# Performance work log

Measured on AMD Instinct MI355X. Metric: run time of the kernel, lower is better.

Reference implementation:

```python
import jax, jax.numpy as jnp
import numpy as np

IN_CH = 64
OUT_CH = 64
SEQ_LEN = 2048
MODES = 64  # modes2 = min(modes1, seq_len//2) = 64
SCALE = 1.0 / (IN_CH * OUT_CH)


def setup_inputs() -> dict:
    key = jax.random.key(0)
    k1, k2, k3 = jax.random.split(key, 3)
    x = jax.random.normal(k1, (32, 8, IN_CH, SEQ_LEN), dtype=jnp.float32)
    # torch.rand(...) complex init scaled by 1/(in*out): real & imag in [0, scale)
    wr = SCALE * jax.random.uniform(k2, (IN_CH, OUT_CH, MODES), dtype=jnp.float32)
    wi = SCALE * jax.random.uniform(k3, (IN_CH, OUT_CH, MODES), dtype=jnp.float32)
    return {"x": x, "wr": wr, "wi": wi}


def reference(x, wr, wi):
    # x: [B, H, E, N] real; weights complex [in, out, modes]
    N = x.shape[-1]
    w = jax.lax.complex(wr, wi)
    x_ft = jnp.fft.rfft(x)                       # [B, H, E, N//2+1] complex64
    a = x_ft[..., :MODES]                        # keep only low modes
    out_low = jnp.einsum('bjix,iox->bjox', a, w)  # per-mode complex matmul
    # zero-fill remaining frequency bins (equivalent to out_ft zeros + slice set)
    pad = N // 2 + 1 - MODES
    out_ft = jnp.pad(out_low, ((0, 0), (0, 0), (0, 0), (0, pad)))
    return jnp.fft.irfft(out_ft, n=N)            # [B, H, out_ch, N] real
```

## Files before the change

### kernel.cpp

```cpp
#include <hip/hip_runtime.h>
#include <hip/hip_bf16.h>


typedef __bf16 bf16x8 __attribute__((ext_vector_type(8)));
typedef float  f32x4  __attribute__((ext_vector_type(4)));

#define SEQ 2048
#define NM2 128
#define KS  2
#define TWO_PI_OVER_N 3.0679615757712823e-03f

__device__ __forceinline__ unsigned int rnbf(float f) {
  unsigned int u = __builtin_bit_cast(unsigned int, f);
  return (u + 0x7fffu + ((u >> 16) & 1u)) >> 16;
}
__device__ __forceinline__ unsigned int pack2(float a, float b) {
  return rnbf(a) | (rnbf(b) << 16);
}
__device__ __forceinline__ float frombf(unsigned int lo16_in_place) {
  return __builtin_bit_cast(float, lo16_in_place);
}

typedef const __attribute__((address_space(1))) unsigned int gu32;
typedef __attribute__((address_space(3))) unsigned int lu32;

__global__ __launch_bounds__(256) void k_tables(unsigned short* __restrict__ t1sw,
                                                unsigned short* __restrict__ t2t) {
  int idx = blockIdx.x * 256 + threadIdx.x;
  int c = idx >> 11;
  int n = idx & 2047;
  int k = c & 63;
  float ph = (float)((k * n) & 2047) * TWO_PI_OVER_N;
  float s, co;
  sincosf(ph, &s, &co);
  float v1 = (c < 64) ? co : -s;
  float ck = (k == 0 ? 1.0f : 2.0f) * (1.0f / 2048.0f);
  float v2 = (c < 64) ? ck * co : -ck * s;
  int kt = n >> 6, part = (n >> 3) & 7, e = n & 7;
  unsigned off = (unsigned)kt * 16384u +
                 (((unsigned)(c * 128 + part * 16)) ^ (((unsigned)c & 7u) << 4)) + 2u * (unsigned)e;
  *(unsigned short*)((char*)t1sw + off) = (unsigned short)rnbf(v1);
  t2t[n * NM2 + c] = (unsigned short)rnbf(v2);
}

__global__ __launch_bounds__(256) void k_gemm1(const float* __restrict__ x,
                                               const unsigned short* __restrict__ t1sw,
                                               unsigned short* __restrict__ P) {
  __shared__ int4 lds4[65536 / 16];
  char* lds = (char*)lds4;
  const int tid = threadIdx.x, wave = tid >> 6, lane = tid & 63;
  const int mtile = blockIdx.x >> 1, ks = blockIdx.x & (KS - 1);
  const int r0 = mtile * 64;
  const int kbase = ks * (SEQ / KS);
  const char* t1base = (const char*)t1sw + (size_t)(kbase >> 6) * 16384;

  const float* xsrc[4];
#pragma unroll
  for (int p = 0; p < 4; ++p) {
    const int row = p * 16 + wave * 4 + (lane >> 4);
    const int u = (lane & 15) ^ (row & 7);
    xsrc[p] = x + (size_t)(r0 + row) * SEQ + kbase + u * 4;
  }

  f32x4 acc[8] = {};

#pragma unroll
  for (int p = 0; p < 4; ++p)
    __builtin_amdgcn_global_load_lds((gu32*)(xsrc[p]),
                                     (lu32*)(lds + p * 4096 + wave * 1024), 16, 0, 0);
#pragma unroll
  for (int p = 0; p < 4; ++p)
    __builtin_amdgcn_global_load_lds((gu32*)(t1base + (p * 256 + tid) * 16),
                                     (lu32*)(lds + 32768 + (p * 256 + wave * 64) * 16), 16, 0, 0);
  asm volatile("s_waitcnt vmcnt(0)" ::: "memory");
  __builtin_amdgcn_s_barrier();

  const int a = wave * 16 + (lane & 15);
  const unsigned xra = (unsigned)(a & 7) << 4;
  const int kg = lane >> 4;

  for (int it = 0; it < 16; ++it) {
    const int cur = it & 1, nxt = cur ^ 1;
    const int xoff = cur * 16384;
    const int toff = 32768 + cur * 16384;
    if (it < 15) {
      const char* tg = t1base + (it + 1) * 16384;
#pragma unroll
      for (int p = 0; p < 4; ++p)
        __builtin_amdgcn_global_load_lds((gu32*)(xsrc[p] + (it + 1) * 64),
                                         (lu32*)(lds + nxt * 16384 + p * 4096 + wave * 1024),
                                         16, 0, 0);
#pragma unroll
      for (int p = 0; p < 4; ++p)
        __builtin_amdgcn_global_load_lds((gu32*)(tg + (p * 256 + tid) * 16),
                                         (lu32*)(lds + 32768 + nxt * 16384 + (p * 256 + wave * 64) * 16),
                                         16, 0, 0);
    }
#pragma unroll
    for (int kss = 0; kss < 2; ++kss) {
      const unsigned byte0 = (unsigned)(a * 256 + kss * 128 + kg * 32);
      const f32x4 lo = *(const f32x4*)(lds + xoff + (byte0 ^ xra));
      const f32x4 hi = *(const f32x4*)(lds + xoff + ((byte0 + 16) ^ xra));
      unsigned c0, c1, c2, c3;
      asm("v_cvt_pk_bf16_f32 %0, %1, %2" : "=v"(c0) : "v"(lo[0]), "v"(lo[1]));
      asm("v_cvt_pk_bf16_f32 %0, %1, %2" : "=v"(c1) : "v"(lo[2]), "v"(lo[3]));
      asm("v_cvt_pk_bf16_f32 %0, %1, %2" : "=v"(c2) : "v"(hi[0]), "v"(hi[1]));
      asm("v_cvt_pk_bf16_f32 %0, %1, %2" : "=v"(c3) : "v"(hi[2]), "v"(hi[3]));
      uint4 pk; pk.x = c0; pk.y = c1; pk.z = c2; pk.w = c3;
      const bf16x8 av = __builtin_bit_cast(bf16x8, pk);
#pragma unroll
      for (int t = 0; t < 8; ++t) {
        const int col = t * 16 + (lane & 15);
        const bf16x8 bv = *(const bf16x8*)(lds + toff +
            ((col * 128 + kss * 64 + kg * 16) ^ ((unsigned)(col & 7) << 4)));
        acc[t] = __builtin_amdgcn_mfma_f32_16x16x32_bf16(av, bv, acc[t], 0, 0, 0);
      }
    }
    asm volatile("s_waitcnt vmcnt(0)" ::: "memory");
    __builtin_amdgcn_s_barrier();
  }
  unsigned short* Pout = P + (size_t)ks * (16384 * NM2);
#pragma unroll
  for (int t = 0; t < 8; ++t) {
    const int col = t * 16 + (lane & 15);
#pragma unroll
    for (int j = 0; j < 4; ++j) {
      const int row = r0 + wave * 16 + (lane >> 4) * 4 + j;
      Pout[row * NM2 + col] = (unsigned short)rnbf(acc[t][j]);
    }
  }
}

__global__ __launch_bounds__(256) void k_stage2(const unsigned short* __restrict__ P,
                                                const float* __restrict__ wr,
                                                const float* __restrict__ wi,
                                                unsigned short* __restrict__ Bx) {
  __shared__ float sA[4][64][64];
  const int b = blockIdx.x;
  const int bjc = b >> 2, oh = (b >> 1) & 1, kh = b & 1;
  const int k0 = kh * 32;
  const int tid = threadIdx.x;
#pragma unroll
  for (int p = 0; p < 16; ++p) {
    int fidx = tid + 256 * p;
    int row_lin = fidx >> 4, q = fidx & 15;
    int col = (q < 8) ? (k0 + q * 4) : (64 + k0 + (q - 8) * 4);
    const unsigned short* base = P + (size_t)(bjc * 256 + row_lin) * NM2 + col;
    f32x4 v = {};
#pragma unroll
    for (int s = 0; s < KS; ++s) {
      uint2 u = *(const uint2*)(base + (size_t)s * (16384 * NM2));
      v[0] += frombf(u.x << 16);
      v[1] += frombf(u.x & 0xffff0000u);
      v[2] += frombf(u.y << 16);
      v[3] += frombf(u.y & 0xffff0000u);
    }
    *(f32x4*)(&sA[row_lin >> 6][row_lin & 63][q * 4]) = v;
  }
  __syncthreads();
  const int o_l = tid >> 3, kg = tid & 7;
  const int o = oh * 32 + o_l;
  const int kb = k0 + kg * 4;
  f32x4 accr[4] = {};
  f32x4 acci[4] = {};
  for (int i = 0; i < 64; ++i) {
    f32x4 wrv = *(const f32x4*)(wr + (i * 64 + o) * 64 + kb);
    f32x4 wiv = *(const f32x4*)(wi + (i * 64 + o) * 64 + kb);
#pragma unroll
    for (int bj = 0; bj < 4; ++bj) {
      f32x4 ar = *(const f32x4*)(&sA[bj][i][kg * 4]);
      f32x4 ai = *(const f32x4*)(&sA[bj][i][32 + kg * 4]);
#pragma unroll
      for (int kk = 0; kk < 4; ++kk) {
        accr[bj][kk] += ar[kk] * wrv[kk] - ai[kk] * wiv[kk];
        acci[bj][kk] += ar[kk] * wiv[kk] + ai[kk] * wrv[kk];
      }
    }
  }
#pragma unroll
  for (int bj = 0; bj < 4; ++bj) {
    const int r = (bjc * 4 + bj) * 64 + o;
    uint2 vr; vr.x = pack2(accr[bj][0], accr[bj][1]); vr.y = pack2(accr[bj][2], accr[bj][3]);
    uint2 vi; vi.x = pack2(acci[bj][0], acci[bj][1]); vi.y = pack2(acci[bj][2], acci[bj][3]);
    *(uint2*)(Bx + r * NM2 + kb)      = vr;
    *(uint2*)(Bx + r * NM2 + 64 + kb) = vi;
  }
}

__global__ __launch_bounds__(256) void k_gemm2(const unsigned short* __restrict__ Bx,
                                               const unsigned short* __restrict__ t2t,
                                               float* __restrict__ out) {
  __shared__ int4 lds4[65536 / 16];
  char* lds = (char*)lds4;
  const int tid = threadIdx.x, wave = tid >> 6, lane = tid & 63;
  const int swz = (blockIdx.x & 7) * 256 + (blockIdx.x >> 3);
  const int mb = swz >> 4, nb = swz & 15;
  const int r0 = mb * 128, n0 = nb * 128;
#pragma unroll
  for (int p = 0; p < 8; ++p) {
    int seg = tid + 256 * p;
    int row = seg >> 4, part = seg & 15;
    unsigned sw = (unsigned)((row * 256 + part * 16) ^ ((row & 7) << 4));
    int4 va = *(const int4*)(Bx + (r0 + row) * NM2 + part * 8);
    *(int4*)(lds + sw) = va;
    int4 vb = *(const int4*)(t2t + (n0 + row) * NM2 + part * 8);
    *(int4*)(lds + 32768 + sw) = vb;
  }
  __syncthreads();
  f32x4 acc[2][8] = {};
#pragma unroll
  for (int ks = 0; ks < 4; ++ks) {
    const int ar0 = wave * 32 + (lane & 15);
    const int ar1 = ar0 + 16;
    const int koff = ks * 64 + (lane >> 4) * 16;
    bf16x8 a0 = *(const bf16x8*)(lds + ((ar0 * 256 + koff) ^ ((unsigned)(ar0 & 7) << 4)));
    bf16x8 a1 = *(const bf16x8*)(lds + ((ar1 * 256 + koff) ^ ((unsigned)(ar1 & 7) << 4)));
#pragma unroll
    for (int t = 0; t < 8; ++t) {
      const int col = t * 16 + (lane & 15);
      bf16x8 bv = *(const bf16x8*)(lds + 32768 + ((col * 256 + koff) ^ ((unsigned)(col & 7) << 4)));
      acc[0][t] = __builtin_amdgcn_mfma_f32_16x16x32_bf16(a0, bv, acc[0][t], 0, 0, 0);
      acc[1][t] = __builtin_amdgcn_mfma_f32_16x16x32_bf16(a1, bv, acc[1][t], 0, 0, 0);
    }
  }
#pragma unroll
  for (int m = 0; m < 2; ++m) {
#pragma unroll
    for (int j = 0; j < 4; ++j) {
      const int row = r0 + wave * 32 + m * 16 + (lane >> 4) * 4 + j;
#pragma unroll
      for (int t = 0; t < 8; ++t) {
        const int col = n0 + t * 16 + (lane & 15);
        out[row * SEQ + col] = acc[m][t][j];
      }
    }
  }
}

extern "C" void kernel_launch(void* const* d_in, const int* in_sizes, int n_in,
                              void* d_out, int out_size, void* d_ws, size_t ws_size,
                              hipStream_t stream) {
  const float* x  = (const float*)d_in[0];
  const float* wr = (const float*)d_in[1];
  const float* wi = (const float*)d_in[2];
  float* out = (float*)d_out;
  char* ws = (char*)d_ws;
  unsigned short* t1sw = (unsigned short*)(ws);
  unsigned short* t2t  = (unsigned short*)(ws + 524288);
  unsigned short* P    = (unsigned short*)(ws + 1048576);
  unsigned short* Bx   = (unsigned short*)(ws + 1048576 + (size_t)KS * 16384 * NM2 * 2);

  k_tables<<<dim3(1024), dim3(256), 0, stream>>>(t1sw, t2t);
  k_gemm1 <<<dim3(256 * KS), dim3(256), 0, stream>>>(x, t1sw, P);
  k_stage2<<<dim3(256),  dim3(256), 0, stream>>>(P, wr, wi, Bx);
  k_gemm2 <<<dim3(2048), dim3(256), 0, stream>>>(Bx, t2t, out);
}
```

Before: 89.93 us.

## Drop split-K in DFT GEMM, retile to 32-row blocks, vectorize output stores

The forward DFT GEMM no longer splits K into two partial products. Each block now covers 32 rows over the full sequence, and the four waves are arranged 2x2, so stage2 reads one bf16 partial instead of summing two and writes less intermediate data. The MFMA operands are swapped so accumulators come out transposed, which allows packed 8-byte stores in gemm1 and 16-byte float4 stores in gemm2 instead of scalar stores. The table kernel uses the hardware v_sin/v_cos instructions on revolutions and writes both cos and sin entries per thread, with half the launch size. Stage2 now runs twice as many blocks, each doing half the work. The hardware sin/cos may be slightly less accurate than sincosf.

```diff
diff --git a/kernel.cpp b/kernel.cpp
--- a/kernel.cpp
+++ b/kernel.cpp
@@ -7,8 +7,6 @@
 
 #define SEQ 2048
 #define NM2 128
-#define KS  2
-#define TWO_PI_OVER_N 3.0679615757712823e-03f
 
 __device__ __forceinline__ unsigned int rnbf(float f) {
   unsigned int u = __builtin_bit_cast(unsigned int, f);
@@ -27,73 +25,73 @@
 __global__ __launch_bounds__(256) void k_tables(unsigned short* __restrict__ t1sw,
                                                 unsigned short* __restrict__ t2t) {
   int idx = blockIdx.x * 256 + threadIdx.x;
-  int c = idx >> 11;
+  int k = idx >> 11;
   int n = idx & 2047;
-  int k = c & 63;
-  float ph = (float)((k * n) & 2047) * TWO_PI_OVER_N;
+  float rev = (float)((k * n) & 2047) * (1.0f / 2048.0f);
   float s, co;
-  sincosf(ph, &s, &co);
-  float v1 = (c < 64) ? co : -s;
+  asm("v_sin_f32 %0, %1" : "=v"(s)  : "v"(rev));
+  asm("v_cos_f32 %0, %1" : "=v"(co) : "v"(rev));
   float ck = (k == 0 ? 1.0f : 2.0f) * (1.0f / 2048.0f);
-  float v2 = (c < 64) ? ck * co : -ck * s;
   int kt = n >> 6, part = (n >> 3) & 7, e = n & 7;
-  unsigned off = (unsigned)kt * 16384u +
-                 (((unsigned)(c * 128 + part * 16)) ^ (((unsigned)c & 7u) << 4)) + 2u * (unsigned)e;
-  *(unsigned short*)((char*)t1sw + off) = (unsigned short)rnbf(v1);
-  t2t[n * NM2 + c] = (unsigned short)rnbf(v2);
+  unsigned base = (unsigned)kt * 16384u + 2u * (unsigned)e;
+  unsigned offc = base + (((unsigned)(k * 128 + part * 16)) ^ (((unsigned)k & 7u) << 4));
+  int c2 = k + 64;
+  unsigned offs = base + (((unsigned)(c2 * 128 + part * 16)) ^ (((unsigned)c2 & 7u) << 4));
+  *(unsigned short*)((char*)t1sw + offc) = (unsigned short)rnbf(co);
+  *(unsigned short*)((char*)t1sw + offs) = (unsigned short)rnbf(-s);
+  t2t[n * NM2 + k]      = (unsigned short)rnbf(ck * co);
+  t2t[n * NM2 + k + 64] = (unsigned short)rnbf(-ck * s);
 }
 
 __global__ __launch_bounds__(256) void k_gemm1(const float* __restrict__ x,
                                                const unsigned short* __restrict__ t1sw,
-                                               unsigned short* __restrict__ P) {
-  __shared__ int4 lds4[65536 / 16];
+                                               unsigned short* __restrict__ A) {
+  __shared__ int4 lds4[49152 / 16];
   char* lds = (char*)lds4;
   const int tid = threadIdx.x, wave = tid >> 6, lane = tid & 63;
-  const int mtile = blockIdx.x >> 1, ks = blockIdx.x & (KS - 1);
-  const int r0 = mtile * 64;
-  const int kbase = ks * (SEQ / KS);
-  const char* t1base = (const char*)t1sw + (size_t)(kbase >> 6) * 16384;
-
-  const float* xsrc[4];
-#pragma unroll
-  for (int p = 0; p < 4; ++p) {
+  const int r0 = blockIdx.x * 32;
+
+  const float* xsrc[2];
+#pragma unroll
+  for (int p = 0; p < 2; ++p) {
     const int row = p * 16 + wave * 4 + (lane >> 4);
     const int u = (lane & 15) ^ (row & 7);
-    xsrc[p] = x + (size_t)(r0 + row) * SEQ + kbase + u * 4;
-  }
-
-  f32x4 acc[8] = {};
-
-#pragma unroll
-  for (int p = 0; p < 4; ++p)
+    xsrc[p] = x + (size_t)(r0 + row) * SEQ + u * 4;
+  }
+
+  f32x4 acc[4] = {};
+
+#pragma unroll
+  for (int p = 0; p < 2; ++p)
     __builtin_amdgcn_global_load_lds((gu32*)(xsrc[p]),
                                      (lu32*)(lds + p * 4096 + wave * 1024), 16, 0, 0);
 #pragma unroll
   for (int p = 0; p < 4; ++p)
-    __builtin_amdgcn_global_load_lds((gu32*)(t1base + (p * 256 + tid) * 16),
-                                     (lu32*)(lds + 32768 + (p * 256 + wave * 64) * 16), 16, 0, 0);
+    __builtin_amdgcn_global_load_lds((gu32*)((const char*)t1sw + (p * 256 + tid) * 16),
+                                     (lu32*)(lds + 16384 + p * 4096 + wave * 1024), 16, 0, 0);
   asm volatile("s_waitcnt vmcnt(0)" ::: "memory");
   __builtin_amdgcn_s_barrier();
 
-  const int a = wave * 16 + (lane & 15);
+  const int wr = wave >> 1, wc = wave & 1;
+  const int a = wr * 16 + (lane & 15);
   const unsigned xra = (unsigned)(a & 7) << 4;
   const int kg = lane >> 4;
 
-  for (int it = 0; it < 16; ++it) {
+  for (int it = 0; it < 32; ++it) {
     const int cur = it & 1, nxt = cur ^ 1;
-    const int xoff = cur * 16384;
-    const int toff = 32768 + cur * 16384;
-    if (it < 15) {
-      const char* tg = t1base + (it + 1) * 16384;
-#pragma unroll
-      for (int p = 0; p < 4; ++p)
+    const int xoff = cur * 8192;
+    const int toff = 16384 + cur * 16384;
+    if (it < 31) {
+      const char* tg = (const char*)t1sw + (size_t)(it + 1) * 16384;
+#pragma unroll
+      for (int p = 0; p < 2; ++p)
         __builtin_amdgcn_global_load_lds((gu32*)(xsrc[p] + (it + 1) * 64),
-                                         (lu32*)(lds + nxt * 16384 + p * 4096 + wave * 1024),
+                                         (lu32*)(lds + nxt * 8192 + p * 4096 + wave * 1024),
                                          16, 0, 0);
 #pragma unroll
       for (int p = 0; p < 4; ++p)
         __builtin_amdgcn_global_load_lds((gu32*)(tg + (p * 256 + tid) * 16),
-                                         (lu32*)(lds + 32768 + nxt * 16384 + (p * 256 + wave * 64) * 16),
+                                         (lu32*)(lds + 16384 + nxt * 16384 + p * 4096 + wave * 1024),
                                          16, 0, 0);
     }
 #pragma unroll
@@ -109,65 +107,59 @@
       uint4 pk; pk.x = c0; pk.y = c1; pk.z = c2; pk.w = c3;
       const bf16x8 av = __builtin_bit_cast(bf16x8, pk);
 #pragma unroll
-      for (int t = 0; t < 8; ++t) {
-        const int col = t * 16 + (lane & 15);
+      for (int t = 0; t < 4; ++t) {
+        const int col = wc * 64 + t * 16 + (lane & 15);
         const bf16x8 bv = *(const bf16x8*)(lds + toff +
             ((col * 128 + kss * 64 + kg * 16) ^ ((unsigned)(col & 7) << 4)));
-        acc[t] = __builtin_amdgcn_mfma_f32_16x16x32_bf16(av, bv, acc[t], 0, 0, 0);
+        acc[t] = __builtin_amdgcn_mfma_f32_16x16x32_bf16(bv, av, acc[t], 0, 0, 0);
       }
     }
     asm volatile("s_waitcnt vmcnt(0)" ::: "memory");
     __builtin_amdgcn_s_barrier();
   }
-  unsigned short* Pout = P + (size_t)ks * (16384 * NM2);
-#pragma unroll
-  for (int t = 0; t < 8; ++t) {
-    const int col = t * 16 + (lane & 15);
-#pragma unroll
-    for (int j = 0; j < 4; ++j) {
-      const int row = r0 + wave * 16 + (lane >> 4) * 4 + j;
-      Pout[row * NM2 + col] = (unsigned short)rnbf(acc[t][j]);
-    }
-  }
-}
-
-__global__ __launch_bounds__(256) void k_stage2(const unsigned short* __restrict__ P,
+  const int row = r0 + wr * 16 + (lane & 15);
+#pragma unroll
+  for (int t = 0; t < 4; ++t) {
+    const int col0 = wc * 64 + t * 16 + kg * 4;
+    uint2 v; v.x = pack2(acc[t][0], acc[t][1]); v.y = pack2(acc[t][2], acc[t][3]);
+    *(uint2*)(A + (size_t)row * NM2 + col0) = v;
+  }
+}
+
+__global__ __launch_bounds__(256) void k_stage2(const unsigned short* __restrict__ A,
                                                 const float* __restrict__ wr,
                                                 const float* __restrict__ wi,
                                                 unsigned short* __restrict__ Bx) {
-  __shared__ float sA[4][64][64];
+  __shared__ float sA[2][64][64];
   const int b = blockIdx.x;
   const int bjc = b >> 2, oh = (b >> 1) & 1, kh = b & 1;
   const int k0 = kh * 32;
   const int tid = threadIdx.x;
 #pragma unroll
-  for (int p = 0; p < 16; ++p) {
+  for (int p = 0; p < 8; ++p) {
     int fidx = tid + 256 * p;
-    int row_lin = fidx >> 4, q = fidx & 15;
-    int col = (q < 8) ? (k0 + q * 4) : (64 + k0 + (q - 8) * 4);
-    const unsigned short* base = P + (size_t)(bjc * 256 + row_lin) * NM2 + col;
-    f32x4 v = {};
-#pragma unroll
-    for (int s = 0; s < KS; ++s) {
-      uint2 u = *(const uint2*)(base + (size_t)s * (16384 * NM2));
-      v[0] += frombf(u.x << 16);
-      v[1] += frombf(u.x & 0xffff0000u);
-      v[2] += frombf(u.y << 16);
-      v[3] += frombf(u.y & 0xffff0000u);
-    }
-    *(f32x4*)(&sA[row_lin >> 6][row_lin & 63][q * 4]) = v;
+    int row = fidx >> 4, q = fidx & 15;
+    int colbf = (q < 8) ? (k0 + q * 4) : (64 + k0 + (q - 8) * 4);
+    uint2 u = *(const uint2*)(A + (size_t)(bjc * 128 + row) * NM2 + colbf);
+    f32x4 v;
+    v[0] = frombf(u.x << 16);
+    v[1] = frombf(u.x & 0xffff0000u);
+    v[2] = frombf(u.y << 16);
+    v[3] = frombf(u.y & 0xffff0000u);
+    int dcol = (q < 8) ? q * 4 : 32 + (q - 8) * 4;
+    *(f32x4*)(&sA[row >> 6][row & 63][dcol]) = v;
   }
   __syncthreads();
-  const int o_l = tid >> 3, kg = tid & 7;
-  const int o = oh * 32 + o_l;
+  const int o = oh * 32 + (tid >> 3);
+  const int kg = tid & 7;
   const int kb = k0 + kg * 4;
-  f32x4 accr[4] = {};
-  f32x4 acci[4] = {};
+  f32x4 accr[2] = {};
+  f32x4 acci[2] = {};
   for (int i = 0; i < 64; ++i) {
     f32x4 wrv = *(const f32x4*)(wr + (i * 64 + o) * 64 + kb);
     f32x4 wiv = *(const f32x4*)(wi + (i * 64 + o) * 64 + kb);
 #pragma unroll
-    for (int bj = 0; bj < 4; ++bj) {
+    for (int bj = 0; bj < 2; ++bj) {
       f32x4 ar = *(const f32x4*)(&sA[bj][i][kg * 4]);
       f32x4 ai = *(const f32x4*)(&sA[bj][i][32 + kg * 4]);
 #pragma unroll
@@ -178,12 +170,12 @@
     }
   }
 #pragma unroll
-  for (int bj = 0; bj < 4; ++bj) {
-    const int r = (bjc * 4 + bj) * 64 + o;
+  for (int bj = 0; bj < 2; ++bj) {
+    const int r = (bjc * 2 + bj) * 64 + o;
     uint2 vr; vr.x = pack2(accr[bj][0], accr[bj][1]); vr.y = pack2(accr[bj][2], accr[bj][3]);
     uint2 vi; vi.x = pack2(acci[bj][0], acci[bj][1]); vi.y = pack2(acci[bj][2], acci[bj][3]);
-    *(uint2*)(Bx + r * NM2 + kb)      = vr;
-    *(uint2*)(Bx + r * NM2 + 64 + kb) = vi;
+    *(uint2*)(Bx + (size_t)r * NM2 + kb)      = vr;
+    *(uint2*)(Bx + (size_t)r * NM2 + 64 + kb) = vi;
   }
 }
 
@@ -201,9 +193,9 @@
     int seg = tid + 256 * p;
     int row = seg >> 4, part = seg & 15;
     unsigned sw = (unsigned)((row * 256 + part * 16) ^ ((row & 7) << 4));
-    int4 va = *(const int4*)(Bx + (r0 + row) * NM2 + part * 8);
+    int4 va = *(const int4*)(Bx + (size_t)(r0 + row) * NM2 + part * 8);
     *(int4*)(lds + sw) = va;
-    int4 vb = *(const int4*)(t2t + (n0 + row) * NM2 + part * 8);
+    int4 vb = *(const int4*)(t2t + (size_t)(n0 + row) * NM2 + part * 8);
     *(int4*)(lds + 32768 + sw) = vb;
   }
   __syncthreads();
@@ -219,20 +211,17 @@
     for (int t = 0; t < 8; ++t) {
       const int col = t * 16 + (lane & 15);
       bf16x8 bv = *(const bf16x8*)(lds + 32768 + ((col * 256 + koff) ^ ((unsigned)(col & 7) << 4)));
-      acc[0][t] = __builtin_amdgcn_mfma_f32_16x16x32_bf16(a0, bv, acc[0][t], 0, 0, 0);
-      acc[1][t] = __builtin_amdgcn_mfma_f32_16x16x32_bf16(a1, bv, acc[1][t], 0, 0, 0);
+      acc[0][t] = __builtin_amdgcn_mfma_f32_16x16x32_bf16(bv, a0, acc[0][t], 0, 0, 0);
+      acc[1][t] = __builtin_amdgcn_mfma_f32_16x16x32_bf16(bv, a1, acc[1][t], 0, 0, 0);
     }
   }
 #pragma unroll
   for (int m = 0; m < 2; ++m) {
-#pragma unroll
-    for (int j = 0; j < 4; ++j) {
-      const int row = r0 + wave * 32 + m * 16 + (lane >> 4) * 4 + j;
-#pragma unroll
-      for (int t = 0; t < 8; ++t) {
-        const int col = n0 + t * 16 + (lane & 15);
-        out[row * SEQ + col] = acc[m][t][j];
-      }
+    const int row = r0 + wave * 32 + m * 16 + (lane & 15);
+#pragma unroll
+    for (int t = 0; t < 8; ++t) {
+      const int col = n0 + t * 16 + (lane >> 4) * 4;
+      *(f32x4*)(out + (size_t)row * SEQ + col) = acc[m][t];
     }
   }
 }
@@ -247,11 +236,11 @@
   char* ws = (char*)d_ws;
   unsigned short* t1sw = (unsigned short*)(ws);
   unsigned short* t2t  = (unsigned short*)(ws + 524288);
-  unsigned short* P    = (unsigned short*)(ws + 1048576);
-  unsigned short* Bx   = (unsigned short*)(ws + 1048576 + (size_t)KS * 16384 * NM2 * 2);
-
-  k_tables<<<dim3(1024), dim3(256), 0, stream>>>(t1sw, t2t);
-  k_gemm1 <<<dim3(256 * KS), dim3(256), 0, stream>>>(x, t1sw, P);
-  k_stage2<<<dim3(256),  dim3(256), 0, stream>>>(P, wr, wi, Bx);
+  unsigned short* A    = (unsigned short*)(ws + 1048576);
+  unsigned short* Bx   = (unsigned short*)(ws + 1048576 + (size_t)16384 * NM2 * 2);
+
+  k_tables<<<dim3(512),  dim3(256), 0, stream>>>(t1sw, t2t);
+  k_gemm1 <<<dim3(512),  dim3(256), 0, stream>>>(x, t1sw, A);
+  k_stage2<<<dim3(512),  dim3(256), 0, stream>>>(A, wr, wi, Bx);
   k_gemm2 <<<dim3(2048), dim3(256), 0, stream>>>(Bx, t2t, out);
 }
```

New measurement: 105.8 us. 17.6% more time.
